# Performance work log

Hardware: AMD Instinct MI355X
Metric: run time of the kernel (lower is better)

Reference implementation:

```python
import jax, jax.numpy as jnp
import numpy as np

TEMPERATURE = 0.1
EPS = 1e-07


def setup_inputs() -> dict:
    key = jax.random.key(0)
    k1, k2 = jax.random.split(key)
    embeddings = jax.random.normal(k1, (4096, 768), dtype=jnp.float32)
    labels = jax.random.normal(k2, (4096, 2), dtype=jnp.float32)
    return {"embeddings": embeddings, "labels": labels}


def _supcr_dim(sims, exp_sims, lab, eps):
    # sims, exp_sims: [M, M]; lab: [M]
    M = lab.shape[0]
    dists = jnp.abs(lab[None, :] - lab[:, None])            # [M, M]
    idx = jnp.argsort(dists, axis=1)                         # row-wise sort order
    sorted_d = jnp.take_along_axis(dists, idx, axis=1)
    sorted_s = jnp.take_along_axis(exp_sims, idx, axis=1)
    # reversed cumsum (suffix sums) along each row
    suffix = jnp.flip(jnp.cumsum(jnp.flip(sorted_s, axis=1), axis=1), axis=1)
    # per-row searchsorted: first index where sorted_d >= dists[i, j]
    pos = jax.vmap(lambda sd, rd: jnp.searchsorted(sd, rd, side='left'))(sorted_d, dists)
    denom = jnp.maximum(jnp.take_along_axis(suffix, pos, axis=1), eps)
    # -log(exp(sims) / denom) == log(denom) - sims
    row_loss = jnp.log(denom) - sims
    off_diag = ~jnp.eye(M, dtype=bool)
    total = jnp.sum(jnp.where(off_diag, row_loss, 0.0))
    return total / (M * (M - 1))


def reference(embeddings, labels):
    # cosine similarity / temperature (torch F.normalize clamps norm at 1e-12)
    norm = jnp.maximum(jnp.linalg.norm(embeddings, axis=1, keepdims=True), 1e-12)
    normed = embeddings / norm
    sims = (normed @ normed.T) / TEMPERATURE                 # [M, M]
    exp_sims = jnp.exp(sims)
    # vmap over label dimensions (labels.T: [num_dims, M])
    losses = jax.vmap(lambda lab: _supcr_dim(sims, exp_sims, lab, EPS))(labels.T)
    return losses
```

## Files before the change

kernel.cpp:

```cpp
#include <hip/hip_runtime.h>
#include <hip/hip_bf16.h>
#include <math.h>

#define MM 4096
#define KK 768
#define NB64 64
#define NBK 2048
#define QSCALE 65536.0f
#define LN2 0.6931471805599453f

typedef short bf16x8 __attribute__((ext_vector_type(8)));
typedef unsigned short u16x8 __attribute__((ext_vector_type(8)));
typedef float f32x4 __attribute__((ext_vector_type(4)));

__device__ __forceinline__ float bf2f(unsigned short u) {
  return __uint_as_float(((unsigned int)u) << 16);
}
__device__ __forceinline__ unsigned short f2bf(float f) {
  __hip_bfloat16 h = __float2bfloat16(f);
  return *(unsigned short*)&h;
}

__device__ __forceinline__ void gload16(const void* g, void* l) {
#if __has_builtin(__builtin_amdgcn_global_load_lds)
  __builtin_amdgcn_global_load_lds((__attribute__((address_space(1))) void*)g,
                                   (__attribute__((address_space(3))) void*)l,
                                   16, 0, 0);
#else
  *(bf16x8*)l = *(const bf16x8*)g;
#endif
}

__global__ __launch_bounds__(256) void knorm(const float* __restrict__ emb,
                                             __hip_bfloat16* __restrict__ nb,
                                             const float* __restrict__ labels,
                                             float* __restrict__ dmm) {
  int row = blockIdx.x;
  int tid = threadIdx.x;
  if (row == MM) {
    float mn0 = 1e30f, mx0 = -1e30f, mn1 = 1e30f, mx1 = -1e30f;
    for (int q = tid; q < MM; q += 256) {
      float2 l2 = ((const float2*)labels)[q];
      mn0 = fminf(mn0, l2.x); mx0 = fmaxf(mx0, l2.x);
      mn1 = fminf(mn1, l2.y); mx1 = fmaxf(mx1, l2.y);
    }
    for (int s = 32; s; s >>= 1) {
      mn0 = fminf(mn0, __shfl_down(mn0, s, 64));
      mx0 = fmaxf(mx0, __shfl_down(mx0, s, 64));
      mn1 = fminf(mn1, __shfl_down(mn1, s, 64));
      mx1 = fmaxf(mx1, __shfl_down(mx1, s, 64));
    }
    __shared__ float redm[4][4];
    if ((tid & 63) == 0) {
      redm[0][tid >> 6] = mn0; redm[1][tid >> 6] = mx0;
      redm[2][tid >> 6] = mn1; redm[3][tid >> 6] = mx1;
    }
    __syncthreads();
    if (tid == 0) {
      dmm[0] = fminf(fminf(redm[0][0], redm[0][1]), fminf(redm[0][2], redm[0][3]));
      dmm[1] = fmaxf(fmaxf(redm[1][0], redm[1][1]), fmaxf(redm[1][2], redm[1][3]));
      dmm[2] = fminf(fminf(redm[2][0], redm[2][1]), fminf(redm[2][2], redm[2][3]));
      dmm[3] = fmaxf(fmaxf(redm[3][0], redm[3][1]), fmaxf(redm[3][2], redm[3][3]));
    }
    return;
  }
  const float* e = emb + (size_t)row * KK;
  float v0 = e[tid], v1 = e[tid + 256], v2 = e[tid + 512];
  float ss = v0 * v0 + v1 * v1 + v2 * v2;
  for (int s = 32; s; s >>= 1) ss += __shfl_down(ss, s, 64);
  __shared__ float red[4];
  if ((tid & 63) == 0) red[tid >> 6] = ss;
  __syncthreads();
  float tot = red[0] + red[1] + red[2] + red[3];
  float inv = 1.f / fmaxf(sqrtf(tot), 1e-12f);
  __hip_bfloat16* o = nb + (size_t)row * KK;
  o[tid] = __float2bfloat16(v0 * inv);
  o[tid + 256] = __float2bfloat16(v1 * inv);
  o[tid + 512] = __float2bfloat16(v2 * inv);
}

union SmemU64 {
  struct { short As[64 * 64]; short Bs[64 * 64]; } s;
  float tbuf[32][68];
};

__global__ __launch_bounds__(256) void kgemm_sym64(const __hip_bfloat16* __restrict__ A,
                                                   unsigned short* __restrict__ out,
                                                   float* __restrict__ srow) {
  __shared__ __align__(16) SmemU64 sm;
  const int tid = threadIdx.x;
  const int w = tid >> 6, l = tid & 63;
  const int wr = w >> 1, wc = w & 1;
  const int b = blockIdx.x;
  int by = (int)((129.0f - sqrtf(16641.0f - 8.0f * (float)b)) * 0.5f);
  by = min(max(by, 0), 63);
  while (by > 0 && (by * (129 - by)) / 2 > b) --by;
  while (by < 63 && (((by + 1) * (129 - (by + 1))) / 2) <= b) ++by;
  const int bx = by + (b - (by * (129 - by)) / 2);
  const int row0 = by * 64, col0 = bx * 64;
  const short* Ag = (const short*)A;

  f32x4 acc[2][2];
#pragma unroll
  for (int mi = 0; mi < 2; ++mi)
#pragma unroll
    for (int ni = 0; ni < 2; ++ni) acc[mi][ni] = (f32x4){0.f, 0.f, 0.f, 0.f};

  const int r0 = tid >> 3, s0 = tid & 7;
  const int sx = ((s0 ^ (r0 & 7)) * 8);
  const int lr = l & 15, kb = (l >> 4) * 8;
  const int xr = (lr & 7) << 3;

  for (int k0 = 0; k0 < KK; k0 += 64) {
    __syncthreads();
    gload16(Ag + (size_t)(row0 + r0) * KK + k0 + sx, &sm.s.As[tid * 8]);
    gload16(Ag + (size_t)(row0 + 32 + r0) * KK + k0 + sx, &sm.s.As[(tid + 256) * 8]);
    gload16(Ag + (size_t)(col0 + r0) * KK + k0 + sx, &sm.s.Bs[tid * 8]);
    gload16(Ag + (size_t)(col0 + 32 + r0) * KK + k0 + sx, &sm.s.Bs[(tid + 256) * 8]);
    __syncthreads();
    bf16x8 av[2][2], bv[2][2];
#pragma unroll
    for (int mi = 0; mi < 2; ++mi)
#pragma unroll
      for (int kh = 0; kh < 2; ++kh)
        av[mi][kh] = *(const bf16x8*)&sm.s.As[(wr * 32 + mi * 16 + lr) * 64 +
                                              ((kh * 32 + kb) ^ xr)];
#pragma unroll
    for (int ni = 0; ni < 2; ++ni)
#pragma unroll
      for (int kh = 0; kh < 2; ++kh)
        bv[ni][kh] = *(const bf16x8*)&sm.s.Bs[(wc * 32 + ni * 16 + lr) * 64 +
                                              ((kh * 32 + kb) ^ xr)];
#pragma unroll
    for (int kh = 0; kh < 2; ++kh)
#pragma unroll
      for (int mi = 0; mi < 2; ++mi)
#pragma unroll
        for (int ni = 0; ni < 2; ++ni)
          acc[mi][ni] = __builtin_amdgcn_mfma_f32_16x16x32_bf16(av[mi][kh], bv[ni][kh],
                                                                acc[mi][ni], 0, 0, 0);
  }

  const int quad = l >> 4;
  const bool diag = (bx == by);

#pragma unroll
  for (int mi = 0; mi < 2; ++mi) {
#pragma unroll
    for (int r = 0; r < 4; ++r) {
      const int grow = row0 + wr * 32 + mi * 16 + quad * 4 + r;
      float rsum = 0.f;
#pragma unroll
      for (int ni = 0; ni < 2; ++ni) {
        const int gcol = col0 + wc * 32 + ni * 16 + lr;
        rsum += (diag && gcol == grow) ? 0.f : acc[mi][ni][r];
      }
#pragma unroll
      for (int mask = 1; mask < 16; mask <<= 1) rsum += __shfl_xor(rsum, mask, 64);
      if (lr == 0) srow[(size_t)grow * 128 + bx * 2 + wc] = rsum / 0.1f;
    }
  }

  if (!diag) {
#pragma unroll
    for (int ni = 0; ni < 2; ++ni) {
      float csum = 0.f;
#pragma unroll
      for (int mi = 0; mi < 2; ++mi)
#pragma unroll
        for (int r = 0; r < 4; ++r) csum += acc[mi][ni][r];
      csum += __shfl_xor(csum, 16, 64);
      csum += __shfl_xor(csum, 32, 64);
      if (quad == 0)
        srow[(size_t)(col0 + wc * 32 + ni * 16 + l) * 128 + by * 2 + wr] = csum / 0.1f;
    }
  }

#pragma unroll
  for (int mi = 0; mi < 2; ++mi)
#pragma unroll
    for (int ni = 0; ni < 2; ++ni)
#pragma unroll
      for (int r = 0; r < 4; ++r)
        acc[mi][ni][r] = __expf(acc[mi][ni][r] / 0.1f);

#pragma unroll
  for (int mi = 0; mi < 2; ++mi)
#pragma unroll
    for (int r = 0; r < 4; ++r) {
      const int grow = row0 + wr * 32 + mi * 16 + quad * 4 + r;
#pragma unroll
      for (int ni = 0; ni < 2; ++ni)
        out[(size_t)grow * MM + col0 + wc * 32 + ni * 16 + lr] = f2bf(acc[mi][ni][r]);
    }

  if (!diag) {
#pragma unroll
    for (int p = 0; p < 2; ++p) {
      __syncthreads();
      if (wc == p) {
#pragma unroll
        for (int ni = 0; ni < 2; ++ni) {
          const int ltr = ni * 16 + lr;
#pragma unroll
          for (int mi = 0; mi < 2; ++mi) {
            const int cbase = wr * 32 + mi * 16 + quad * 4;
#pragma unroll
            for (int r = 0; r < 4; ++r)
              sm.tbuf[ltr][cbase + r] = acc[mi][ni][r];
          }
        }
      }
      __syncthreads();
      const int trow = tid >> 3;
      const int cseg = (tid & 7) * 8;
      const int gtr = col0 + p * 32 + trow;
      u16x8 vv;
#pragma unroll
      for (int q = 0; q < 8; ++q) vv[q] = f2bf(sm.tbuf[trow][cseg + q]);
      *(u16x8*)(out + (size_t)gtr * MM + row0 + cseg) = vv;
    }
  }
}

__global__ __launch_bounds__(256) void kgemm(const __hip_bfloat16* __restrict__ A,
                                             int rowBase,
                                             unsigned short* __restrict__ out,
                                             float* __restrict__ srow) {
  __shared__ __align__(16) short As[128 * 32];
  __shared__ __align__(16) short Bs[128 * 32];
  const int tid = threadIdx.x;
  const int w = tid >> 6, l = tid & 63;
  const int wr = w >> 1, wc = w & 1;
  const int bx = blockIdx.x;
  const int row0 = rowBase + blockIdx.y * 128;
  const int col0 = bx * 128;
  const short* Ag = (const short*)A;

  f32x4 acc[4][4];
#pragma unroll
  for (int mi = 0; mi < 4; ++mi)
#pragma unroll
    for (int ni = 0; ni < 4; ++ni) acc[mi][ni] = (f32x4){0.f, 0.f, 0.f, 0.f};

  const int r0 = tid >> 2, s0 = tid & 3;
  const int r1 = (tid + 256) >> 2;
  const int lrow = l & 15, kb = (l >> 4) * 8;

  for (int k0 = 0; k0 < KK; k0 += 32) {
    __syncthreads();
    gload16(Ag + (size_t)(row0 + r0) * KK + k0 + s0 * 8, &As[tid * 8]);
    gload16(Ag + (size_t)(row0 + r1) * KK + k0 + s0 * 8, &As[(tid + 256) * 8]);
    gload16(Ag + (size_t)(col0 + r0) * KK + k0 + s0 * 8, &Bs[tid * 8]);
    gload16(Ag + (size_t)(col0 + r1) * KK + k0 + s0 * 8, &Bs[(tid + 256) * 8]);
    __syncthreads();
    bf16x8 av[4], bv[4];
#pragma unroll
    for (int mi = 0; mi < 4; ++mi)
      av[mi] = *(const bf16x8*)&As[(wr * 64 + mi * 16 + lrow) * 32 + kb];
#pragma unroll
    for (int ni = 0; ni < 4; ++ni)
      bv[ni] = *(const bf16x8*)&Bs[(wc * 64 + ni * 16 + lrow) * 32 + kb];
#pragma unroll
    for (int mi = 0; mi < 4; ++mi)
#pragma unroll
      for (int ni = 0; ni < 4; ++ni)
        acc[mi][ni] = __builtin_amdgcn_mfma_f32_16x16x32_bf16(av[mi], bv[ni],
                                                              acc[mi][ni], 0, 0, 0);
  }

  const int quad = l >> 4;
#pragma unroll
  for (int mi = 0; mi < 4; ++mi) {
#pragma unroll
    for (int r = 0; r < 4; ++r) {
      const int grow = row0 + wr * 64 + mi * 16 + quad * 4 + r;
      float rsum = 0.f;
#pragma unroll
      for (int ni = 0; ni < 4; ++ni) {
        const int gcol = col0 + wc * 64 + ni * 16 + lrow;
        float a = acc[mi][ni][r];
        out[(size_t)(grow - rowBase) * MM + gcol] = f2bf(__expf(a / 0.1f));
        rsum += (gcol == grow) ? 0.f : a;
      }
#pragma unroll
      for (int mask = 1; mask < 16; mask <<= 1) rsum += __shfl_xor(rsum, mask, 64);
      if (lrow == 0) srow[(size_t)grow * 128 + bx * 2 + wc] = rsum / 0.1f;
    }
  }
}

__global__ __launch_bounds__(256) void kloss(const unsigned short* __restrict__ expb,
                                             int rowBase,
                                             const float* __restrict__ labels,
                                             const float* __restrict__ dmm,
                                             float* __restrict__ part_logd) {
  const int i = rowBase + blockIdx.x;
  const unsigned short* row = expb + (size_t)blockIdx.x * MM;
  __shared__ __align__(16) unsigned int histU[NBK];
  __shared__ unsigned int wsumU[4];
  __shared__ float red[4];
  const int tid = threadIdx.x;
  const int lane = tid & 63, wid = tid >> 6;
  const int m0 = tid * 16;
  const int b0 = tid * 8;

  unsigned int gq[16];
  {
    u16x8 a = *(const u16x8*)(row + m0);
    u16x8 bq = *(const u16x8*)(row + m0 + 8);
#pragma unroll
    for (int u = 0; u < 8; ++u) {
      gq[u] = (unsigned int)(bf2f(a[u]) * QSCALE + 0.5f);
      gq[u + 8] = (unsigned int)(bf2f(bq[u]) * QSCALE + 0.5f);
    }
  }
  float lx[16], ly[16];
  {
    const float4* lp4 = (const float4*)(labels + (size_t)m0 * 2);
#pragma unroll
    for (int q = 0; q < 8; ++q) {
      float4 v4 = lp4[q];
      lx[2 * q] = v4.x; ly[2 * q] = v4.y;
      lx[2 * q + 1] = v4.z; ly[2 * q + 1] = v4.w;
    }
  }
  const float c0 = labels[(size_t)i * 2], c1 = labels[(size_t)i * 2 + 1];

  for (int d = 0; d < 2; ++d) {
    __syncthreads();
    ((uint4*)histU)[tid] = (uint4){0, 0, 0, 0};
    ((uint4*)histU)[tid + 256] = (uint4){0, 0, 0, 0};
    __syncthreads();

    const float c = d ? c1 : c0;
    const float dmin = dmm[2 * d], dmax = dmm[2 * d + 1];
    const float tmax = fmaxf(fmaxf(c - dmin, dmax - c), 1e-30f);
    const float scale = (float)NBK / tmax;

    int bidx[16];
#pragma unroll
    for (int u = 0; u < 16; ++u) {
      const float t = fabsf((d ? ly[u] : lx[u]) - c);
      int bk = (int)(t * scale);
      bk = min(bk, NBK - 1);
      bidx[u] = bk;
      atomicAdd(&histU[bk], gq[u]);
    }
    __syncthreads();

    unsigned int hh[8];
    {
      uint4 ha = *(const uint4*)&histU[b0];
      uint4 hb = *(const uint4*)&histU[b0 + 4];
      hh[0] = ha.x; hh[1] = ha.y; hh[2] = ha.z; hh[3] = ha.w;
      hh[4] = hb.x; hh[5] = hb.y; hh[6] = hb.z; hh[7] = hb.w;
    }
    unsigned int S = 0;
#pragma unroll
    for (int u = 0; u < 8; ++u) S += hh[u];
    unsigned int v = S;
#pragma unroll
    for (int s = 1; s < 64; s <<= 1) {
      unsigned int t2 = __shfl_down(v, s, 64);
      if (lane + s < 64) v += t2;
    }
    if (lane == 0) wsumU[wid] = v;
    __syncthreads();
    unsigned int woff = 0;
#pragma unroll
    for (int q = 0; q < 4; ++q) woff += (q > wid) ? wsumU[q] : 0u;
    unsigned int run = woff + (v - S);
#pragma unroll
    for (int u = 7; u >= 0; --u) {
      run += hh[u];
      hh[u] = run;
    }
    {
      uint4 oa = {hh[0], hh[1], hh[2], hh[3]};
      uint4 ob = {hh[4], hh[5], hh[6], hh[7]};
      *(uint4*)&histU[b0] = oa;
      *(uint4*)&histU[b0 + 4] = ob;
    }
    __syncthreads();

    float mprod = 1.f;
    int esum = 0;
#pragma unroll
    for (int u = 0; u < 16; ++u) {
      const float df = (float)histU[bidx[u]];
      int ex;
      const float mant = frexpf(df, &ex);
      mprod *= mant;
      esum += ex;
    }
    float acc = __logf(mprod) + (float)(esum - 256) * LN2;

    for (int s = 32; s; s >>= 1) acc += __shfl_down(acc, s, 64);
    __syncthreads();
    if ((tid & 63) == 0) red[tid >> 6] = acc;
    __syncthreads();
    if (tid == 0) {
      const float tf = (float)(wsumU[0] + wsumU[1] + wsumU[2] + wsumU[3]);
      part_logd[d * MM + i] =
          red[0] + red[1] + red[2] + red[3] - (__logf(tf) - 16.f * LN2);
    }
  }
}

__global__ __launch_bounds__(256) void kred1(const float* __restrict__ part_logd,
                                             const float* __restrict__ srow,
                                             double* __restrict__ red3) {
  const int tid = threadIdx.x;
  const int base = blockIdx.x * 64;
  double ss = 0.0, s0 = 0.0, s1 = 0.0;
  for (int q = tid; q < 64 * 128; q += 256)
    ss += (double)srow[(size_t)base * 128 + q];
  if (tid < 64) {
    s0 = (double)part_logd[base + tid];
    s1 = (double)part_logd[MM + base + tid];
  }
  for (int s = 32; s; s >>= 1) {
    s0 += __shfl_down(s0, s, 64);
    s1 += __shfl_down(s1, s, 64);
    ss += __shfl_down(ss, s, 64);
  }
  __shared__ double red[3][4];
  if ((tid & 63) == 0) {
    red[0][tid >> 6] = s0; red[1][tid >> 6] = s1; red[2][tid >> 6] = ss;
  }
  __syncthreads();
  if (tid == 0) {
    red3[blockIdx.x * 3 + 0] = red[0][0] + red[0][1] + red[0][2] + red[0][3];
    red3[blockIdx.x * 3 + 1] = red[1][0] + red[1][1] + red[1][2] + red[1][3];
    red3[blockIdx.x * 3 + 2] = red[2][0] + red[2][1] + red[2][2] + red[2][3];
  }
}

__global__ __launch_bounds__(64) void kred2(const double* __restrict__ red3,
                                            float* __restrict__ out) {
  const int t = threadIdx.x;
  double s0 = red3[t * 3 + 0], s1 = red3[t * 3 + 1], ss = red3[t * 3 + 2];
  for (int s = 32; s; s >>= 1) {
    s0 += __shfl_down(s0, s, 64);
    s1 += __shfl_down(s1, s, 64);
    ss += __shfl_down(ss, s, 64);
  }
  if (t == 0) {
    const double n = (double)MM * (double)(MM - 1);
    out[0] = (float)((s0 - ss) / n);
    out[1] = (float)((s1 - ss) / n);
  }
}

extern "C" void kernel_launch(void* const* d_in, const int* in_sizes, int n_in,
                              void* d_out, int out_size, void* d_ws, size_t ws_size,
                              hipStream_t stream) {
  const float* emb = (const float*)d_in[0];
  const float* labels = (const float*)d_in[1];
  float* out = (float*)d_out;
  char* ws = (char*)d_ws;

  size_t off = 0;
  auto alloc = [&](size_t bytes) {
    void* p = ws + off;
    off = (off + bytes + 255) & ~(size_t)255;
    return p;
  };
  __hip_bfloat16* nb = (__hip_bfloat16*)alloc((size_t)MM * KK * 2);
  float* dmm = (float*)alloc(4 * 4);
  float* part_logd = (float*)alloc((size_t)2 * MM * 4);
  float* srow = (float*)alloc((size_t)MM * 128 * 4);
  double* red3 = (double*)alloc((size_t)64 * 3 * 8);
  size_t fixed = off;

  size_t avail = (ws_size > fixed) ? (ws_size - fixed) : 0;
  long long cr = (long long)(avail / ((size_t)MM * 2));
  cr = (cr / 128) * 128;
  if (cr > MM) cr = MM;
  if (cr < 128) cr = 128;
  int chunk_rows = (int)cr;
  unsigned short* expb = (unsigned short*)(ws + fixed);

  knorm<<<MM + 1, 256, 0, stream>>>(emb, nb, labels, dmm);

  if (chunk_rows == MM) {
    kgemm_sym64<<<NB64 * (NB64 + 1) / 2, 256, 0, stream>>>(nb, expb, srow);
    kloss<<<MM, 256, 0, stream>>>(expb, 0, labels, dmm, part_logd);
  } else {
    hipMemsetAsync(srow, 0, (size_t)MM * 128 * 4, stream);
    for (int base = 0; base < MM; base += chunk_rows) {
      int rows = MM - base < chunk_rows ? MM - base : chunk_rows;
      kgemm<<<dim3(MM / 128, rows / 128), 256, 0, stream>>>(nb, base, expb, srow);
      kloss<<<rows, 256, 0, stream>>>(expb, base, labels, dmm, part_logd);
    }
  }
  kred1<<<64, 256, 0, stream>>>(part_logd, srow, red3);
  kred2<<<1, 64, 0, stream>>>(red3, out);
}
```

Measured before the change: 81.58 us.

## Enlarge symmetric GEMM tiles to 128x128 with 512 threads and swizzled block order

The symmetric similarity GEMM moves from 64x64 tiles with 256 threads to 128x128 tiles with 512 threads (8 waves, each computing a 64x32 sub-tile). Block indices are remapped with a stride-66 interleave across the 528 upper-triangular tiles, and srow slots are re-indexed, with unused slots zero-filled to keep the 128-wide layout. Larger tiles raise operand reuse and halve the global reloads of the normalized embeddings. In exchange they use more LDS and registers, and with only 528 blocks the GPU may be less evenly loaded.

```diff
diff --git a/kernel.cpp b/kernel.cpp
--- a/kernel.cpp
+++ b/kernel.cpp
@@ -4,7 +4,7 @@
 
 #define MM 4096
 #define KK 768
-#define NB64 64
+#define NBT 32
 #define NBK 2048
 #define QSCALE 65536.0f
 #define LN2 0.6931471805599453f
@@ -79,76 +79,74 @@
   o[tid + 512] = __float2bfloat16(v2 * inv);
 }
 
-union SmemU64 {
-  struct { short As[64 * 64]; short Bs[64 * 64]; } s;
-  float tbuf[32][68];
+union SmemU {
+  struct { short As[128 * 64]; short Bs[128 * 64]; } s;
+  float tbuf[32][132];
 };
 
-__global__ __launch_bounds__(256) void kgemm_sym64(const __hip_bfloat16* __restrict__ A,
-                                                   unsigned short* __restrict__ out,
-                                                   float* __restrict__ srow) {
-  __shared__ __align__(16) SmemU64 sm;
+__global__ __launch_bounds__(512, 4) void kgemm_sym128(
+    const __hip_bfloat16* __restrict__ A,
+    unsigned short* __restrict__ out,
+    float* __restrict__ srow) {
+  __shared__ __align__(16) SmemU sm;
   const int tid = threadIdx.x;
   const int w = tid >> 6, l = tid & 63;
-  const int wr = w >> 1, wc = w & 1;
-  const int b = blockIdx.x;
-  int by = (int)((129.0f - sqrtf(16641.0f - 8.0f * (float)b)) * 0.5f);
-  by = min(max(by, 0), 63);
-  while (by > 0 && (by * (129 - by)) / 2 > b) --by;
-  while (by < 63 && (((by + 1) * (129 - (by + 1))) / 2) <= b) ++by;
-  const int bx = by + (b - (by * (129 - by)) / 2);
-  const int row0 = by * 64, col0 = bx * 64;
+  const int wr = w >> 2, wc = w & 3;
+  int b = blockIdx.x;
+  b = (b & 7) * 66 + (b >> 3);
+  int by = (int)((65.0f - sqrtf(4225.0f - 8.0f * (float)b)) * 0.5f);
+  by = min(max(by, 0), NBT - 1);
+  while (by > 0 && (by * (65 - by)) / 2 > b) --by;
+  while (by < NBT - 1 && (((by + 1) * (65 - (by + 1))) / 2) <= b) ++by;
+  const int bx = by + (b - (by * (65 - by)) / 2);
+  const int row0 = by * 128, col0 = bx * 128;
   const short* Ag = (const short*)A;
 
-  f32x4 acc[2][2];
-#pragma unroll
-  for (int mi = 0; mi < 2; ++mi)
+  f32x4 acc[4][2];
+#pragma unroll
+  for (int mi = 0; mi < 4; ++mi)
 #pragma unroll
     for (int ni = 0; ni < 2; ++ni) acc[mi][ni] = (f32x4){0.f, 0.f, 0.f, 0.f};
 
   const int r0 = tid >> 3, s0 = tid & 7;
   const int sx = ((s0 ^ (r0 & 7)) * 8);
-  const int lr = l & 15, kb = (l >> 4) * 8;
+  const int lr = l & 15, kb = (l >> 4) * 8, quad = l >> 4;
   const int xr = (lr & 7) << 3;
 
   for (int k0 = 0; k0 < KK; k0 += 64) {
     __syncthreads();
     gload16(Ag + (size_t)(row0 + r0) * KK + k0 + sx, &sm.s.As[tid * 8]);
-    gload16(Ag + (size_t)(row0 + 32 + r0) * KK + k0 + sx, &sm.s.As[(tid + 256) * 8]);
+    gload16(Ag + (size_t)(row0 + 64 + r0) * KK + k0 + sx, &sm.s.As[(tid + 512) * 8]);
     gload16(Ag + (size_t)(col0 + r0) * KK + k0 + sx, &sm.s.Bs[tid * 8]);
-    gload16(Ag + (size_t)(col0 + 32 + r0) * KK + k0 + sx, &sm.s.Bs[(tid + 256) * 8]);
-    __syncthreads();
-    bf16x8 av[2][2], bv[2][2];
-#pragma unroll
-    for (int mi = 0; mi < 2; ++mi)
-#pragma unroll
-      for (int kh = 0; kh < 2; ++kh)
-        av[mi][kh] = *(const bf16x8*)&sm.s.As[(wr * 32 + mi * 16 + lr) * 64 +
-                                              ((kh * 32 + kb) ^ xr)];
-#pragma unroll
-    for (int ni = 0; ni < 2; ++ni)
-#pragma unroll
-      for (int kh = 0; kh < 2; ++kh)
-        bv[ni][kh] = *(const bf16x8*)&sm.s.Bs[(wc * 32 + ni * 16 + lr) * 64 +
-                                              ((kh * 32 + kb) ^ xr)];
-#pragma unroll
-    for (int kh = 0; kh < 2; ++kh)
-#pragma unroll
-      for (int mi = 0; mi < 2; ++mi)
+    gload16(Ag + (size_t)(col0 + 64 + r0) * KK + k0 + sx, &sm.s.Bs[(tid + 512) * 8]);
+    __syncthreads();
+#pragma unroll
+    for (int kh = 0; kh < 2; ++kh) {
+      bf16x8 av[4], bv[2];
+#pragma unroll
+      for (int mi = 0; mi < 4; ++mi)
+        av[mi] = *(const bf16x8*)&sm.s.As[(wr * 64 + mi * 16 + lr) * 64 +
+                                          ((kh * 32 + kb) ^ xr)];
+#pragma unroll
+      for (int ni = 0; ni < 2; ++ni)
+        bv[ni] = *(const bf16x8*)&sm.s.Bs[(wc * 32 + ni * 16 + lr) * 64 +
+                                          ((kh * 32 + kb) ^ xr)];
+#pragma unroll
+      for (int mi = 0; mi < 4; ++mi)
 #pragma unroll
         for (int ni = 0; ni < 2; ++ni)
-          acc[mi][ni] = __builtin_amdgcn_mfma_f32_16x16x32_bf16(av[mi][kh], bv[ni][kh],
+          acc[mi][ni] = __builtin_amdgcn_mfma_f32_16x16x32_bf16(av[mi], bv[ni],
                                                                 acc[mi][ni], 0, 0, 0);
-  }
-
-  const int quad = l >> 4;
+    }
+  }
+
   const bool diag = (bx == by);
 
 #pragma unroll
-  for (int mi = 0; mi < 2; ++mi) {
+  for (int mi = 0; mi < 4; ++mi) {
 #pragma unroll
     for (int r = 0; r < 4; ++r) {
-      const int grow = row0 + wr * 32 + mi * 16 + quad * 4 + r;
+      const int grow = row0 + wr * 64 + mi * 16 + quad * 4 + r;
       float rsum = 0.f;
 #pragma unroll
       for (int ni = 0; ni < 2; ++ni) {
@@ -157,7 +155,7 @@
       }
 #pragma unroll
       for (int mask = 1; mask < 16; mask <<= 1) rsum += __shfl_xor(rsum, mask, 64);
-      if (lr == 0) srow[(size_t)grow * 128 + bx * 2 + wc] = rsum / 0.1f;
+      if (lr == 0) srow[(size_t)grow * 128 + bx * 4 + wc] = rsum / 0.1f;
     }
   }
 
@@ -166,18 +164,21 @@
     for (int ni = 0; ni < 2; ++ni) {
       float csum = 0.f;
 #pragma unroll
-      for (int mi = 0; mi < 2; ++mi)
+      for (int mi = 0; mi < 4; ++mi)
 #pragma unroll
         for (int r = 0; r < 4; ++r) csum += acc[mi][ni][r];
       csum += __shfl_xor(csum, 16, 64);
       csum += __shfl_xor(csum, 32, 64);
-      if (quad == 0)
-        srow[(size_t)(col0 + wc * 32 + ni * 16 + l) * 128 + by * 2 + wr] = csum / 0.1f;
-    }
-  }
-
-#pragma unroll
-  for (int mi = 0; mi < 2; ++mi)
+      if (quad == 0) {
+        const size_t rowi = (size_t)(col0 + wc * 32 + ni * 16 + l);
+        srow[rowi * 128 + by * 4 + wr] = csum / 0.1f;
+        srow[rowi * 128 + by * 4 + 2 + wr] = 0.f;
+      }
+    }
+  }
+
+#pragma unroll
+  for (int mi = 0; mi < 4; ++mi)
 #pragma unroll
     for (int ni = 0; ni < 2; ++ni)
 #pragma unroll
@@ -185,10 +186,10 @@
         acc[mi][ni][r] = __expf(acc[mi][ni][r] / 0.1f);
 
 #pragma unroll
-  for (int mi = 0; mi < 2; ++mi)
+  for (int mi = 0; mi < 4; ++mi)
 #pragma unroll
     for (int r = 0; r < 4; ++r) {
-      const int grow = row0 + wr * 32 + mi * 16 + quad * 4 + r;
+      const int grow = row0 + wr * 64 + mi * 16 + quad * 4 + r;
 #pragma unroll
       for (int ni = 0; ni < 2; ++ni)
         out[(size_t)grow * MM + col0 + wc * 32 + ni * 16 + lr] = f2bf(acc[mi][ni][r]);
@@ -196,15 +197,15 @@
 
   if (!diag) {
 #pragma unroll
-    for (int p = 0; p < 2; ++p) {
+    for (int p = 0; p < 4; ++p) {
       __syncthreads();
       if (wc == p) {
 #pragma unroll
         for (int ni = 0; ni < 2; ++ni) {
           const int ltr = ni * 16 + lr;
 #pragma unroll
-          for (int mi = 0; mi < 2; ++mi) {
-            const int cbase = wr * 32 + mi * 16 + quad * 4;
+          for (int mi = 0; mi < 4; ++mi) {
+            const int cbase = wr * 64 + mi * 16 + quad * 4;
 #pragma unroll
             for (int r = 0; r < 4; ++r)
               sm.tbuf[ltr][cbase + r] = acc[mi][ni][r];
@@ -212,8 +213,8 @@
         }
       }
       __syncthreads();
-      const int trow = tid >> 3;
-      const int cseg = (tid & 7) * 8;
+      const int trow = tid >> 4;
+      const int cseg = (tid & 15) * 8;
       const int gtr = col0 + p * 32 + trow;
       u16x8 vv;
 #pragma unroll
@@ -485,7 +486,7 @@
   knorm<<<MM + 1, 256, 0, stream>>>(emb, nb, labels, dmm);
 
   if (chunk_rows == MM) {
-    kgemm_sym64<<<NB64 * (NB64 + 1) / 2, 256, 0, stream>>>(nb, expb, srow);
+    kgemm_sym128<<<NBT * (NBT + 1) / 2, 512, 0, stream>>>(nb, expb, srow);
     kloss<<<MM, 256, 0, stream>>>(expb, 0, labels, dmm, part_logd);
   } else {
     hipMemsetAsync(srow, 0, (size_t)MM * 128 * 4, stream);
```

After: 89.61 us. 1.1x slower.

## Fuse both label-dimension histograms in loss kernel and swizzle GEMM block order

Applied to the files above, without the earlier changes.

The loss kernel now builds both label dimensions' bucket histograms in one pass, using a doubled shared-memory histogram and a single combined suffix scan. This replaces two sequential passes, each with its own zeroing, scan and barriers. Bucket indices are packed into 16-bit halves to save registers. Separately, the symmetric GEMM remaps block indices with a stride-260 swizzle so concurrently scheduled blocks land on different triangular tiles, which may change L2 locality or XCD distribution. The costs are twice the LDS per block, which may lower occupancy, and a scan that relies on each pair of waves covering exactly one dimension.

```diff
diff --git a/kernel.cpp b/kernel.cpp
--- a/kernel.cpp
+++ b/kernel.cpp
@@ -91,7 +91,8 @@
   const int tid = threadIdx.x;
   const int w = tid >> 6, l = tid & 63;
   const int wr = w >> 1, wc = w & 1;
-  const int b = blockIdx.x;
+  int b = blockIdx.x;
+  b = (b & 7) * 260 + (b >> 3);
   int by = (int)((129.0f - sqrtf(16641.0f - 8.0f * (float)b)) * 0.5f);
   by = min(max(by, 0), 63);
   while (by > 0 && (by * (129 - by)) / 2 > b) --by;
@@ -297,13 +298,13 @@
                                              float* __restrict__ part_logd) {
   const int i = rowBase + blockIdx.x;
   const unsigned short* row = expb + (size_t)blockIdx.x * MM;
-  __shared__ __align__(16) unsigned int histU[NBK];
+  __shared__ __align__(16) unsigned int histU[2 * NBK];
   __shared__ unsigned int wsumU[4];
-  __shared__ float red[4];
+  __shared__ float red[2][4];
   const int tid = threadIdx.x;
   const int lane = tid & 63, wid = tid >> 6;
   const int m0 = tid * 16;
-  const int b0 = tid * 8;
+  const int b0 = tid * 16;
 
   unsigned int gq[16];
   {
@@ -315,96 +316,100 @@
       gq[u + 8] = (unsigned int)(bf2f(bq[u]) * QSCALE + 0.5f);
     }
   }
-  float lx[16], ly[16];
+  const float c0 = labels[(size_t)i * 2], c1 = labels[(size_t)i * 2 + 1];
+  const float tmax0 = fmaxf(fmaxf(c0 - dmm[0], dmm[1] - c0), 1e-30f);
+  const float tmax1 = fmaxf(fmaxf(c1 - dmm[2], dmm[3] - c1), 1e-30f);
+  const float scale0 = (float)NBK / tmax0;
+  const float scale1 = (float)NBK / tmax1;
+
+  ((uint4*)histU)[tid] = (uint4){0, 0, 0, 0};
+  ((uint4*)histU)[tid + 256] = (uint4){0, 0, 0, 0};
+  ((uint4*)histU)[tid + 512] = (uint4){0, 0, 0, 0};
+  ((uint4*)histU)[tid + 768] = (uint4){0, 0, 0, 0};
+  __syncthreads();
+
+  unsigned int bpack[16];
   {
     const float4* lp4 = (const float4*)(labels + (size_t)m0 * 2);
 #pragma unroll
     for (int q = 0; q < 8; ++q) {
       float4 v4 = lp4[q];
-      lx[2 * q] = v4.x; ly[2 * q] = v4.y;
-      lx[2 * q + 1] = v4.z; ly[2 * q + 1] = v4.w;
-    }
-  }
-  const float c0 = labels[(size_t)i * 2], c1 = labels[(size_t)i * 2 + 1];
-
-  for (int d = 0; d < 2; ++d) {
-    __syncthreads();
-    ((uint4*)histU)[tid] = (uint4){0, 0, 0, 0};
-    ((uint4*)histU)[tid + 256] = (uint4){0, 0, 0, 0};
-    __syncthreads();
-
-    const float c = d ? c1 : c0;
-    const float dmin = dmm[2 * d], dmax = dmm[2 * d + 1];
-    const float tmax = fmaxf(fmaxf(c - dmin, dmax - c), 1e-30f);
-    const float scale = (float)NBK / tmax;
-
-    int bidx[16];
-#pragma unroll
-    for (int u = 0; u < 16; ++u) {
-      const float t = fabsf((d ? ly[u] : lx[u]) - c);
-      int bk = (int)(t * scale);
-      bk = min(bk, NBK - 1);
-      bidx[u] = bk;
-      atomicAdd(&histU[bk], gq[u]);
-    }
-    __syncthreads();
-
-    unsigned int hh[8];
-    {
-      uint4 ha = *(const uint4*)&histU[b0];
-      uint4 hb = *(const uint4*)&histU[b0 + 4];
-      hh[0] = ha.x; hh[1] = ha.y; hh[2] = ha.z; hh[3] = ha.w;
-      hh[4] = hb.x; hh[5] = hb.y; hh[6] = hb.z; hh[7] = hb.w;
-    }
-    unsigned int S = 0;
-#pragma unroll
-    for (int u = 0; u < 8; ++u) S += hh[u];
-    unsigned int v = S;
-#pragma unroll
-    for (int s = 1; s < 64; s <<= 1) {
-      unsigned int t2 = __shfl_down(v, s, 64);
-      if (lane + s < 64) v += t2;
-    }
-    if (lane == 0) wsumU[wid] = v;
-    __syncthreads();
-    unsigned int woff = 0;
-#pragma unroll
-    for (int q = 0; q < 4; ++q) woff += (q > wid) ? wsumU[q] : 0u;
-    unsigned int run = woff + (v - S);
-#pragma unroll
-    for (int u = 7; u >= 0; --u) {
-      run += hh[u];
-      hh[u] = run;
-    }
-    {
-      uint4 oa = {hh[0], hh[1], hh[2], hh[3]};
-      uint4 ob = {hh[4], hh[5], hh[6], hh[7]};
-      *(uint4*)&histU[b0] = oa;
-      *(uint4*)&histU[b0 + 4] = ob;
-    }
-    __syncthreads();
-
-    float mprod = 1.f;
-    int esum = 0;
-#pragma unroll
-    for (int u = 0; u < 16; ++u) {
-      const float df = (float)histU[bidx[u]];
-      int ex;
-      const float mant = frexpf(df, &ex);
-      mprod *= mant;
-      esum += ex;
-    }
-    float acc = __logf(mprod) + (float)(esum - 256) * LN2;
-
-    for (int s = 32; s; s >>= 1) acc += __shfl_down(acc, s, 64);
-    __syncthreads();
-    if ((tid & 63) == 0) red[tid >> 6] = acc;
-    __syncthreads();
-    if (tid == 0) {
-      const float tf = (float)(wsumU[0] + wsumU[1] + wsumU[2] + wsumU[3]);
-      part_logd[d * MM + i] =
-          red[0] + red[1] + red[2] + red[3] - (__logf(tf) - 16.f * LN2);
-    }
+      const float ta = fabsf(v4.x - c0), tb = fabsf(v4.y - c1);
+      const float tc2 = fabsf(v4.z - c0), td = fabsf(v4.w - c1);
+      int a0 = min((int)(ta * scale0), NBK - 1);
+      int a1 = min((int)(tb * scale1), NBK - 1);
+      int b02 = min((int)(tc2 * scale0), NBK - 1);
+      int b1 = min((int)(td * scale1), NBK - 1);
+      bpack[2 * q] = (unsigned int)a0 | ((unsigned int)a1 << 16);
+      bpack[2 * q + 1] = (unsigned int)b02 | ((unsigned int)b1 << 16);
+      atomicAdd(&histU[a0], gq[2 * q]);
+      atomicAdd(&histU[NBK + a1], gq[2 * q]);
+      atomicAdd(&histU[b02], gq[2 * q + 1]);
+      atomicAdd(&histU[NBK + b1], gq[2 * q + 1]);
+    }
+  }
+  __syncthreads();
+
+  unsigned int hh[16];
+#pragma unroll
+  for (int q2 = 0; q2 < 4; ++q2) {
+    uint4 ha = *(const uint4*)&histU[b0 + 4 * q2];
+    hh[4 * q2 + 0] = ha.x; hh[4 * q2 + 1] = ha.y;
+    hh[4 * q2 + 2] = ha.z; hh[4 * q2 + 3] = ha.w;
+  }
+  unsigned int S = 0;
+#pragma unroll
+  for (int u = 0; u < 16; ++u) S += hh[u];
+  unsigned int v = S;
+#pragma unroll
+  for (int s = 1; s < 64; s <<= 1) {
+    unsigned int t2 = __shfl_down(v, s, 64);
+    if (lane + s < 64) v += t2;
+  }
+  if (lane == 0) wsumU[wid] = v;
+  __syncthreads();
+  unsigned int woff = (wid == 0) ? wsumU[1] : ((wid == 2) ? wsumU[3] : 0u);
+  unsigned int run = woff + (v - S);
+#pragma unroll
+  for (int u = 15; u >= 0; --u) {
+    run += hh[u];
+    hh[u] = run;
+  }
+#pragma unroll
+  for (int q2 = 0; q2 < 4; ++q2) {
+    uint4 oa = {hh[4 * q2], hh[4 * q2 + 1], hh[4 * q2 + 2], hh[4 * q2 + 3]};
+    *(uint4*)&histU[b0 + 4 * q2] = oa;
+  }
+  __syncthreads();
+
+  float mp0 = 1.f, mp1 = 1.f;
+  int e0 = 0, e1 = 0;
+#pragma unroll
+  for (int u = 0; u < 16; ++u) {
+    const int bk0 = (int)(bpack[u] & 0xFFFFu);
+    const int bk1 = (int)(bpack[u] >> 16);
+    int ex;
+    float mant = frexpf((float)histU[bk0], &ex);
+    mp0 *= mant; e0 += ex;
+    mant = frexpf((float)histU[NBK + bk1], &ex);
+    mp1 *= mant; e1 += ex;
+  }
+  float a0 = __logf(mp0) + (float)(e0 - 256) * LN2;
+  float a1 = __logf(mp1) + (float)(e1 - 256) * LN2;
+
+  for (int s = 32; s; s >>= 1) {
+    a0 += __shfl_down(a0, s, 64);
+    a1 += __shfl_down(a1, s, 64);
+  }
+  if (lane == 0) { red[0][wid] = a0; red[1][wid] = a1; }
+  __syncthreads();
+  if (tid == 0) {
+    const float tf0 = (float)(wsumU[0] + wsumU[1]);
+    const float tf1 = (float)(wsumU[2] + wsumU[3]);
+    part_logd[i] = red[0][0] + red[0][1] + red[0][2] + red[0][3] -
+                   (__logf(tf0) - 16.f * LN2);
+    part_logd[MM + i] = red[1][0] + red[1][1] + red[1][2] + red[1][3] -
+                        (__logf(tf1) - 16.f * LN2);
   }
 }
 
```

Measured after the change: 82.95 us. Within noise of the previous version (+1.7%).

## Fuse both label dims into one packed 64-bit histogram pass in kloss

Applied to the files above, without the earlier changes.

The loss kernel now builds histograms for both label dimensions in a single pass. Each bin is a 64-bit shared-memory word that packs the quantized exp-sum in the low half and an element count in the high half. The per-element lookup of suffix sums is replaced by a per-bin term, count times log2 of the suffix, computed during the scan, which removes a sync round and the second loop over dimensions. Bin count per dimension is halved to 1024 so both histograms fit in shared memory, which makes the distance quantization coarser and may shift accuracy.

```diff
diff --git a/kernel.cpp b/kernel.cpp
--- a/kernel.cpp
+++ b/kernel.cpp
@@ -5,7 +5,7 @@
 #define MM 4096
 #define KK 768
 #define NB64 64
-#define NBK 2048
+#define NBK 1024
 #define QSCALE 65536.0f
 #define LN2 0.6931471805599453f
 
@@ -297,114 +297,88 @@
                                              float* __restrict__ part_logd) {
   const int i = rowBase + blockIdx.x;
   const unsigned short* row = expb + (size_t)blockIdx.x * MM;
-  __shared__ __align__(16) unsigned int histU[NBK];
-  __shared__ unsigned int wsumU[4];
-  __shared__ float red[4];
+  __shared__ __align__(16) unsigned long long histU[2 * NBK];
+  __shared__ unsigned long long wsumU[4];
+  __shared__ float redf[4];
   const int tid = threadIdx.x;
   const int lane = tid & 63, wid = tid >> 6;
   const int m0 = tid * 16;
   const int b0 = tid * 8;
 
-  unsigned int gq[16];
+  const float c0 = labels[(size_t)i * 2], c1 = labels[(size_t)i * 2 + 1];
+  const float tmax0 = fmaxf(fmaxf(c0 - dmm[0], dmm[1] - c0), 1e-30f);
+  const float tmax1 = fmaxf(fmaxf(c1 - dmm[2], dmm[3] - c1), 1e-30f);
+  const float scale0 = (float)NBK / tmax0;
+  const float scale1 = (float)NBK / tmax1;
+
+#pragma unroll
+  for (int q = 0; q < 4; ++q)
+    ((uint4*)histU)[tid + 256 * q] = (uint4){0, 0, 0, 0};
+  __syncthreads();
+
   {
     u16x8 a = *(const u16x8*)(row + m0);
     u16x8 bq = *(const u16x8*)(row + m0 + 8);
-#pragma unroll
-    for (int u = 0; u < 8; ++u) {
-      gq[u] = (unsigned int)(bf2f(a[u]) * QSCALE + 0.5f);
-      gq[u + 8] = (unsigned int)(bf2f(bq[u]) * QSCALE + 0.5f);
-    }
-  }
-  float lx[16], ly[16];
-  {
     const float4* lp4 = (const float4*)(labels + (size_t)m0 * 2);
 #pragma unroll
     for (int q = 0; q < 8; ++q) {
       float4 v4 = lp4[q];
-      lx[2 * q] = v4.x; ly[2 * q] = v4.y;
-      lx[2 * q + 1] = v4.z; ly[2 * q + 1] = v4.w;
-    }
-  }
-  const float c0 = labels[(size_t)i * 2], c1 = labels[(size_t)i * 2 + 1];
-
-  for (int d = 0; d < 2; ++d) {
-    __syncthreads();
-    ((uint4*)histU)[tid] = (uint4){0, 0, 0, 0};
-    ((uint4*)histU)[tid + 256] = (uint4){0, 0, 0, 0};
-    __syncthreads();
-
-    const float c = d ? c1 : c0;
-    const float dmin = dmm[2 * d], dmax = dmm[2 * d + 1];
-    const float tmax = fmaxf(fmaxf(c - dmin, dmax - c), 1e-30f);
-    const float scale = (float)NBK / tmax;
-
-    int bidx[16];
-#pragma unroll
-    for (int u = 0; u < 16; ++u) {
-      const float t = fabsf((d ? ly[u] : lx[u]) - c);
-      int bk = (int)(t * scale);
-      bk = min(bk, NBK - 1);
-      bidx[u] = bk;
-      atomicAdd(&histU[bk], gq[u]);
-    }
-    __syncthreads();
-
-    unsigned int hh[8];
-    {
-      uint4 ha = *(const uint4*)&histU[b0];
-      uint4 hb = *(const uint4*)&histU[b0 + 4];
-      hh[0] = ha.x; hh[1] = ha.y; hh[2] = ha.z; hh[3] = ha.w;
-      hh[4] = hb.x; hh[5] = hb.y; hh[6] = hb.z; hh[7] = hb.w;
-    }
-    unsigned int S = 0;
-#pragma unroll
-    for (int u = 0; u < 8; ++u) S += hh[u];
-    unsigned int v = S;
-#pragma unroll
-    for (int s = 1; s < 64; s <<= 1) {
-      unsigned int t2 = __shfl_down(v, s, 64);
-      if (lane + s < 64) v += t2;
-    }
-    if (lane == 0) wsumU[wid] = v;
-    __syncthreads();
-    unsigned int woff = 0;
-#pragma unroll
-    for (int q = 0; q < 4; ++q) woff += (q > wid) ? wsumU[q] : 0u;
-    unsigned int run = woff + (v - S);
-#pragma unroll
-    for (int u = 7; u >= 0; --u) {
-      run += hh[u];
-      hh[u] = run;
-    }
-    {
-      uint4 oa = {hh[0], hh[1], hh[2], hh[3]};
-      uint4 ob = {hh[4], hh[5], hh[6], hh[7]};
-      *(uint4*)&histU[b0] = oa;
-      *(uint4*)&histU[b0 + 4] = ob;
-    }
-    __syncthreads();
-
-    float mprod = 1.f;
-    int esum = 0;
-#pragma unroll
-    for (int u = 0; u < 16; ++u) {
-      const float df = (float)histU[bidx[u]];
-      int ex;
-      const float mant = frexpf(df, &ex);
-      mprod *= mant;
-      esum += ex;
-    }
-    float acc = __logf(mprod) + (float)(esum - 256) * LN2;
-
-    for (int s = 32; s; s >>= 1) acc += __shfl_down(acc, s, 64);
-    __syncthreads();
-    if ((tid & 63) == 0) red[tid >> 6] = acc;
-    __syncthreads();
-    if (tid == 0) {
-      const float tf = (float)(wsumU[0] + wsumU[1] + wsumU[2] + wsumU[3]);
-      part_logd[d * MM + i] =
-          red[0] + red[1] + red[2] + red[3] - (__logf(tf) - 16.f * LN2);
-    }
+      const unsigned short r0u = (2 * q < 8) ? a[2 * q] : bq[2 * q - 8];
+      const unsigned short r1u = (2 * q + 1 < 8) ? a[2 * q + 1] : bq[2 * q + 1 - 8];
+      const unsigned long long g0 =
+          (unsigned long long)(unsigned int)(bf2f(r0u) * QSCALE + 0.5f) | (1ULL << 32);
+      const unsigned long long g1 =
+          (unsigned long long)(unsigned int)(bf2f(r1u) * QSCALE + 0.5f) | (1ULL << 32);
+      const int a0 = min((int)(fabsf(v4.x - c0) * scale0), NBK - 1);
+      const int a1 = min((int)(fabsf(v4.y - c1) * scale1), NBK - 1);
+      const int b2 = min((int)(fabsf(v4.z - c0) * scale0), NBK - 1);
+      const int b3 = min((int)(fabsf(v4.w - c1) * scale1), NBK - 1);
+      atomicAdd(&histU[a0], g0);
+      atomicAdd(&histU[NBK + a1], g0);
+      atomicAdd(&histU[b2], g1);
+      atomicAdd(&histU[NBK + b3], g1);
+    }
+  }
+  __syncthreads();
+
+  unsigned long long hh[8];
+#pragma unroll
+  for (int q = 0; q < 4; ++q) {
+    uint4 t4 = *(const uint4*)&histU[b0 + 2 * q];
+    hh[2 * q] = (unsigned long long)t4.x | ((unsigned long long)t4.y << 32);
+    hh[2 * q + 1] = (unsigned long long)t4.z | ((unsigned long long)t4.w << 32);
+  }
+  unsigned long long S = 0;
+#pragma unroll
+  for (int u = 0; u < 8; ++u) S += hh[u];
+  unsigned long long v = S;
+#pragma unroll
+  for (int s = 1; s < 64; s <<= 1) {
+    unsigned long long t2 = __shfl_down(v, s, 64);
+    if (lane + s < 64) v += t2;
+  }
+  if (lane == 0) wsumU[wid] = v;
+  __syncthreads();
+  unsigned long long woff = (wid == 0) ? wsumU[1] : ((wid == 2) ? wsumU[3] : 0ULL);
+  unsigned long long run = woff + (v - S);
+
+  float acc2 = 0.f;
+#pragma unroll
+  for (int u = 7; u >= 0; --u) {
+    run += hh[u];
+    const float nf = (float)(unsigned int)(hh[u] >> 32);
+    const float sufq = (float)(unsigned int)run;
+    acc2 += nf * __log2f(fmaxf(sufq, 1.f));
+  }
+
+  for (int s = 32; s; s >>= 1) acc2 += __shfl_down(acc2, s, 64);
+  if (lane == 0) redf[wid] = acc2;
+  __syncthreads();
+  if (tid == 0) {
+    const float tf0 = (float)(unsigned int)(wsumU[0] + wsumU[1]);
+    const float tf1 = (float)(unsigned int)(wsumU[2] + wsumU[3]);
+    part_logd[i] = (redf[0] + redf[1] - 65536.f - __log2f(tf0) + 16.f) * LN2;
+    part_logd[MM + i] = (redf[2] + redf[3] - 65536.f - __log2f(tf1) + 16.f) * LN2;
   }
 }
 
```

After: 77.93 us. 4.5% less time.
